# Performance work log

Hardware: AMD Instinct MI355X
Metric: run time of the kernel (lower is better)

The kernel has to match this reference:

```python
import jax, jax.numpy as jnp
import numpy as np

K = 32  # attention rank
EPS = 1e-6

def setup_inputs() -> dict:
    key = jax.random.key(0)
    k1, k2 = jax.random.split(key)
    N, d = 500000, 256
    x = jax.random.normal(k1, (N, d), dtype=jnp.float32)
    # Xavier-normal-ish scale for Linear(d, 4k)
    W = jax.random.normal(k2, (d, 4 * K), dtype=jnp.float32) * jnp.sqrt(2.0 / (d + 4 * K))
    b = jnp.zeros((4 * K,), dtype=jnp.float32)
    return {"x": x, "W": W, "b": b}

def reference(x, W, b):
    # X = ReLU(x @ W + b): [N, 4k]
    X = jax.nn.relu(x @ W + b)
    U = X[:, :K]            # [N, k]
    V = X[:, K:2 * K]       # [N, k]
    Z = X[:, 2 * K:3 * K]   # [N, k]
    T = X[:, 3 * K:]        # [N, k]
    # joint_normalize2: norm_factor = sum(U @ (V^T @ ones)) / N + eps
    s = V.sum(axis=0)                              # [k] == V^T @ ones
    norm_factor = (U @ s).sum() / U.shape[0] + EPS  # scalar
    D = 1.0 / norm_factor
    # low-rank attention: U @ (V^T @ Z), inner [k, k] GEMM kept tiny
    VtZ = jnp.einsum('nk,nj->kj', V, Z)  # [k, k]
    res = U @ VtZ                        # [N, k]
    return jnp.concatenate((res * D, T), axis=1)  # [N, 2k]
```

## Files before the change

kernel.cpp:

```cpp
#include <hip/hip_runtime.h>
#include <hip/hip_bf16.h>

#define DK 256
#define NC 128
#define EPSV 1e-6f

typedef __bf16 bf16x8 __attribute__((ext_vector_type(8)));
typedef float f32x4 __attribute__((ext_vector_type(4)));


__global__ __launch_bounds__(512, 2) void k_gemm(
    const float* __restrict__ x, const float* __restrict__ W,
    const float* __restrict__ bias, float* __restrict__ out,
    float* __restrict__ accg, int N)
{
  __shared__ float Vs[64 * 36];
  __shared__ float Zs[64 * 36];
  __shared__ float redS[64];

  const int tid  = threadIdx.x;
  const int wave = tid >> 6;
  const int lane = tid & 63;
  const int quad = lane >> 4;
  const int l16  = lane & 15;
  const int mw   = wave >> 1;
  const int nw   = wave & 1;

  bf16x8 Bf[8][4];
  float bias4[4];
  #pragma unroll
  for (int ntl = 0; ntl < 4; ++ntl) {
    const int n = nw * 64 + ntl * 16 + l16;
    bias4[ntl] = bias[n];
    #pragma unroll
    for (int kk = 0; kk < 8; ++kk) {
      const int k0 = kk * 32 + quad * 8;
      bf16x8 f;
      #pragma unroll
      for (int j = 0; j < 8; ++j) f[j] = (__bf16)W[(size_t)(k0 + j) * NC + n];
      Bf[kk][ntl] = f;
    }
  }

  float usumv[2] = {0.f, 0.f};
  float ssumv[2] = {0.f, 0.f};
  const int cell = tid >> 1;
  const int rh   = tid & 1;
  const int ck   = cell >> 3;
  const int cj   = (cell & 7) * 4;
  float vtz[4] = {0.f, 0.f, 0.f, 0.f};

  const int nchunks = (N + 63) >> 6;
  for (int c = blockIdx.x; c < nchunks; c += gridDim.x) {
    const int rbase = c * 64;
    const int arow  = rbase + mw * 16 + l16;
    const bool rv   = arow < N;
    const float* xr = x + (size_t)arow * DK;

    f32x4 acc[4];
    #pragma unroll
    for (int t = 0; t < 4; ++t) acc[t] = (f32x4){0.f, 0.f, 0.f, 0.f};

    #pragma unroll
    for (int kk = 0; kk < 8; ++kk) {
      const int koff = kk * 32 + quad * 8;
      f32x4 a0 = {0.f,0.f,0.f,0.f}, a1 = {0.f,0.f,0.f,0.f};
      if (rv) {
        a0 = *(const f32x4*)(xr + koff);
        a1 = *(const f32x4*)(xr + koff + 4);
      }
      bf16x8 af;
      af[0] = (__bf16)a0.x; af[1] = (__bf16)a0.y;
      af[2] = (__bf16)a0.z; af[3] = (__bf16)a0.w;
      af[4] = (__bf16)a1.x; af[5] = (__bf16)a1.y;
      af[6] = (__bf16)a1.z; af[7] = (__bf16)a1.w;
      #pragma unroll
      for (int ntl = 0; ntl < 4; ++ntl)
        acc[ntl] = __builtin_amdgcn_mfma_f32_16x16x32_bf16(af, Bf[kk][ntl], acc[ntl], 0, 0, 0);
    }

    #pragma unroll
    for (int ntl = 0; ntl < 4; ++ntl) {
      #pragma unroll
      for (int r = 0; r < 4; ++r) {
        const int lrow = mw * 16 + quad * 4 + r;
        const int grow = rbase + lrow;
        const bool ok = grow < N;
        float v = acc[ntl][r] + bias4[ntl];
        v = fmaxf(v, 0.f);
        if (!ok) v = 0.f;
        if (nw == 0) {
          if (ntl < 2) {
            if (ok) out[(size_t)grow * 64 + ntl * 16 + l16] = v;
            usumv[ntl] += v;
          } else {
            ssumv[ntl - 2] += v;
            Vs[lrow * 36 + (ntl - 2) * 16 + l16] = v;
          }
        } else {
          if (ntl < 2) {
            Zs[lrow * 36 + ntl * 16 + l16] = v;
          } else {
            if (ok) out[(size_t)grow * 64 + 32 + (ntl - 2) * 16 + l16] = v;
          }
        }
      }
    }
    __syncthreads();
    const int rr0 = rh * 32;
    #pragma unroll 4
    for (int r = rr0; r < rr0 + 32; ++r) {
      const float vv = Vs[r * 36 + ck];
      vtz[0] += vv * Zs[r * 36 + cj + 0];
      vtz[1] += vv * Zs[r * 36 + cj + 1];
      vtz[2] += vv * Zs[r * 36 + cj + 2];
      vtz[3] += vv * Zs[r * 36 + cj + 3];
    }
    __syncthreads();
  }

  if (tid < 64) redS[tid] = 0.f;
  __syncthreads();
  if (nw == 0) {
    atomicAdd(&redS[l16],      usumv[0]);
    atomicAdd(&redS[16 + l16], usumv[1]);
    atomicAdd(&redS[32 + l16], ssumv[0]);
    atomicAdd(&redS[48 + l16], ssumv[1]);
  }
  __syncthreads();
  if (tid < 64) atomicAdd(&accg[tid], redS[tid]);
  atomicAdd(&accg[64 + ck * 32 + cj + 0], vtz[0]);
  atomicAdd(&accg[64 + ck * 32 + cj + 1], vtz[1]);
  atomicAdd(&accg[64 + ck * 32 + cj + 2], vtz[2]);
  atomicAdd(&accg[64 + ck * 32 + cj + 3], vtz[3]);
}

__global__ void k_norm(float* __restrict__ accg, int N) {
  const int t = threadIdx.x;
  float p = 0.f;
  if (t < 32) p = accg[t] * accg[32 + t];
  #pragma unroll
  for (int off = 16; off >= 1; off >>= 1) p += __shfl_down(p, off);
  if (t == 0) accg[1088] = 1.0f / (p / (float)N + EPSV);
}

__global__ __launch_bounds__(256) void k_res(float* __restrict__ out,
                                             const float* __restrict__ accg, int N) {
  __shared__ float Ms[32 * 33];
  __shared__ float Us[64 * 33];
  const float D = accg[1088];
  for (int i = threadIdx.x; i < 1024; i += 256)
    Ms[(i >> 5) * 33 + (i & 31)] = accg[64 + i] * D;
  __syncthreads();
  const int j  = threadIdx.x & 31;
  const int r0 = threadIdx.x >> 5;
  const int ngroups = (N + 63) >> 6;
  for (int g = blockIdx.x; g < ngroups; g += gridDim.x) {
    const int rbase = g * 64;
    #pragma unroll
    for (int i = 0; i < 8; ++i) {
      const int lr = r0 + i * 8;
      const int row = rbase + lr;
      Us[lr * 33 + j] = (row < N) ? out[(size_t)row * 64 + j] : 0.f;
    }
    __syncthreads();
    #pragma unroll
    for (int i = 0; i < 8; ++i) {
      const int lr = r0 + i * 8;
      const int row = rbase + lr;
      if (row < N) {
        float a = 0.f;
        #pragma unroll
        for (int k = 0; k < 32; ++k) a += Us[lr * 33 + k] * Ms[k * 33 + j];
        out[(size_t)row * 64 + j] = a;
      }
    }
    __syncthreads();
  }
}

extern "C" void kernel_launch(void* const* d_in, const int* in_sizes, int n_in,
                              void* d_out, int out_size, void* d_ws, size_t ws_size,
                              hipStream_t stream) {
  const float* x    = (const float*)d_in[0];
  const float* W    = (const float*)d_in[1];
  const float* b    = (const float*)d_in[2];
  float* out  = (float*)d_out;
  float* accg = (float*)d_ws;
  const int N = in_sizes[0] / DK;

  hipMemsetAsync(accg, 0, 1089 * sizeof(float), stream);
  hipLaunchKernelGGL(k_gemm, dim3(256),  dim3(512), 0, stream, x, W, b, out, accg, N);
  hipLaunchKernelGGL(k_norm, dim3(1),    dim3(64),  0, stream, accg, N);
  hipLaunchKernelGGL(k_res,  dim3(1024), dim3(256), 0, stream, out, accg, N);
}
```

Baseline: 946.8 us.

## Stage W in LDS, batch x loads, compute VtZ with MFMA, one block per k_res group

Moves the bf16 copy of W out of per-thread registers into shared memory so the GEMM kernel uses fewer registers. This lets it request more resident blocks and doubles the grid. All x loads for a row chunk are now issued before the conversions and MFMAs, to expose more memory-level parallelism. The V^T·Z accumulation switches from scalar FMAs to bf16 MFMA on transposed shared-memory tiles, which loses some precision. The residual kernel now launches one block per 64-row group instead of a grid-stride loop. Shared memory per block rises to about 64KB, which may cap the actual occupancy gain.

```diff
diff --git a/kernel.cpp b/kernel.cpp
--- a/kernel.cpp
+++ b/kernel.cpp
@@ -6,17 +6,19 @@
 #define EPSV 1e-6f
 
 typedef __bf16 bf16x8 __attribute__((ext_vector_type(8)));
+typedef __bf16 bf16x4 __attribute__((ext_vector_type(4)));
 typedef float f32x4 __attribute__((ext_vector_type(4)));
 
 
-__global__ __launch_bounds__(512, 2) void k_gemm(
+__global__ __launch_bounds__(512, 4) void k_gemm(
     const float* __restrict__ x, const float* __restrict__ W,
     const float* __restrict__ bias, float* __restrict__ out,
     float* __restrict__ accg, int N)
 {
-  __shared__ float Vs[64 * 36];
-  __shared__ float Zs[64 * 36];
-  __shared__ float redS[64];
+  __shared__ __bf16 Wlds[32768];
+  __shared__ __bf16 Vt[32 * 72];
+  __shared__ __bf16 Zt[32 * 72];
+  __shared__ float  redS[64];
 
   const int tid  = threadIdx.x;
   const int wave = tid >> 6;
@@ -26,95 +28,110 @@
   const int mw   = wave >> 1;
   const int nw   = wave & 1;
 
-  bf16x8 Bf[8][4];
+  for (int f = tid; f < 4096; f += 512) {
+    const int n  = f & 127;
+    const int qk = f >> 7;
+    const int k0 = (qk >> 2) * 32 + (qk & 3) * 8;
+    bf16x8 w;
+    #pragma unroll
+    for (int j = 0; j < 8; ++j) w[j] = (__bf16)W[(size_t)(k0 + j) * NC + n];
+    *(bf16x8*)&Wlds[f * 8] = w;
+  }
   float bias4[4];
   #pragma unroll
-  for (int ntl = 0; ntl < 4; ++ntl) {
-    const int n = nw * 64 + ntl * 16 + l16;
-    bias4[ntl] = bias[n];
-    #pragma unroll
-    for (int kk = 0; kk < 8; ++kk) {
-      const int k0 = kk * 32 + quad * 8;
-      bf16x8 f;
-      #pragma unroll
-      for (int j = 0; j < 8; ++j) f[j] = (__bf16)W[(size_t)(k0 + j) * NC + n];
-      Bf[kk][ntl] = f;
-    }
-  }
+  for (int ntl = 0; ntl < 4; ++ntl) bias4[ntl] = bias[nw * 64 + ntl * 16 + l16];
+  __syncthreads();
 
   float usumv[2] = {0.f, 0.f};
   float ssumv[2] = {0.f, 0.f};
-  const int cell = tid >> 1;
-  const int rh   = tid & 1;
-  const int ck   = cell >> 3;
-  const int cj   = (cell & 7) * 4;
-  float vtz[4] = {0.f, 0.f, 0.f, 0.f};
+  f32x4 vacc = (f32x4){0.f, 0.f, 0.f, 0.f};
+  const int mt = wave >> 1, nt = wave & 1;
 
   const int nchunks = (N + 63) >> 6;
   for (int c = blockIdx.x; c < nchunks; c += gridDim.x) {
-    const int rbase = c * 64;
+    const int rbase = c << 6;
     const int arow  = rbase + mw * 16 + l16;
     const bool rv   = arow < N;
     const float* xr = x + (size_t)arow * DK;
 
-    f32x4 acc[4];
-    #pragma unroll
-    for (int t = 0; t < 4; ++t) acc[t] = (f32x4){0.f, 0.f, 0.f, 0.f};
-
+    f32x4 xv[16];
     #pragma unroll
     for (int kk = 0; kk < 8; ++kk) {
       const int koff = kk * 32 + quad * 8;
-      f32x4 a0 = {0.f,0.f,0.f,0.f}, a1 = {0.f,0.f,0.f,0.f};
-      if (rv) {
-        a0 = *(const f32x4*)(xr + koff);
-        a1 = *(const f32x4*)(xr + koff + 4);
-      }
+      xv[2 * kk]     = rv ? *(const f32x4*)(xr + koff)     : (f32x4){0.f,0.f,0.f,0.f};
+      xv[2 * kk + 1] = rv ? *(const f32x4*)(xr + koff + 4) : (f32x4){0.f,0.f,0.f,0.f};
+    }
+
+    f32x4 acc[4];
+    #pragma unroll
+    for (int t = 0; t < 4; ++t) acc[t] = (f32x4){0.f, 0.f, 0.f, 0.f};
+
+    #pragma unroll
+    for (int kk = 0; kk < 8; ++kk) {
       bf16x8 af;
-      af[0] = (__bf16)a0.x; af[1] = (__bf16)a0.y;
-      af[2] = (__bf16)a0.z; af[3] = (__bf16)a0.w;
-      af[4] = (__bf16)a1.x; af[5] = (__bf16)a1.y;
-      af[6] = (__bf16)a1.z; af[7] = (__bf16)a1.w;
-      #pragma unroll
-      for (int ntl = 0; ntl < 4; ++ntl)
-        acc[ntl] = __builtin_amdgcn_mfma_f32_16x16x32_bf16(af, Bf[kk][ntl], acc[ntl], 0, 0, 0);
+      af[0] = (__bf16)xv[2*kk].x;   af[1] = (__bf16)xv[2*kk].y;
+      af[2] = (__bf16)xv[2*kk].z;   af[3] = (__bf16)xv[2*kk].w;
+      af[4] = (__bf16)xv[2*kk+1].x; af[5] = (__bf16)xv[2*kk+1].y;
+      af[6] = (__bf16)xv[2*kk+1].z; af[7] = (__bf16)xv[2*kk+1].w;
+      #pragma unroll
+      for (int ntl = 0; ntl < 4; ++ntl) {
+        const bf16x8 bf = *(const bf16x8*)&Wlds[(((kk << 2) | quad) * 128
+                                                + nw * 64 + ntl * 16 + l16) * 8];
+        acc[ntl] = __builtin_amdgcn_mfma_f32_16x16x32_bf16(af, bf, acc[ntl], 0, 0, 0);
+      }
     }
 
     #pragma unroll
     for (int ntl = 0; ntl < 4; ++ntl) {
+      float v4[4];
       #pragma unroll
       for (int r = 0; r < 4; ++r) {
-        const int lrow = mw * 16 + quad * 4 + r;
-        const int grow = rbase + lrow;
-        const bool ok = grow < N;
+        const int grow = rbase + mw * 16 + quad * 4 + r;
         float v = acc[ntl][r] + bias4[ntl];
         v = fmaxf(v, 0.f);
-        if (!ok) v = 0.f;
-        if (nw == 0) {
-          if (ntl < 2) {
-            if (ok) out[(size_t)grow * 64 + ntl * 16 + l16] = v;
-            usumv[ntl] += v;
-          } else {
-            ssumv[ntl - 2] += v;
-            Vs[lrow * 36 + (ntl - 2) * 16 + l16] = v;
+        if (grow >= N) v = 0.f;
+        v4[r] = v;
+      }
+      const int grow0 = rbase + mw * 16 + quad * 4;
+      if (nw == 0) {
+        if (ntl < 2) {
+          #pragma unroll
+          for (int r = 0; r < 4; ++r) {
+            if (grow0 + r < N) out[(size_t)(grow0 + r) * 64 + ntl * 16 + l16] = v4[r];
+            usumv[ntl] += v4[r];
           }
         } else {
-          if (ntl < 2) {
-            Zs[lrow * 36 + ntl * 16 + l16] = v;
-          } else {
-            if (ok) out[(size_t)grow * 64 + 32 + (ntl - 2) * 16 + l16] = v;
-          }
+          ssumv[ntl - 2] += v4[0] + v4[1] + v4[2] + v4[3];
+          bf16x4 pv;
+          pv[0] = (__bf16)v4[0]; pv[1] = (__bf16)v4[1];
+          pv[2] = (__bf16)v4[2]; pv[3] = (__bf16)v4[3];
+          const int col = (ntl - 2) * 16 + l16;
+          const int lrow = mw * 16 + quad * 4;
+          *(bf16x4*)&Vt[col * 72 + lrow] = pv;
         }
+      } else {
+        if (ntl < 2) {
+          bf16x4 pv;
+          pv[0] = (__bf16)v4[0]; pv[1] = (__bf16)v4[1];
+          pv[2] = (__bf16)v4[2]; pv[3] = (__bf16)v4[3];
+          const int col = ntl * 16 + l16;
+          const int lrow = mw * 16 + quad * 4;
+          *(bf16x4*)&Zt[col * 72 + lrow] = pv;
+        } else {
+          #pragma unroll
+          for (int r = 0; r < 4; ++r)
+            if (grow0 + r < N) out[(size_t)(grow0 + r) * 64 + 32 + (ntl - 2) * 16 + l16] = v4[r];
+        }
       }
     }
     __syncthreads();
-    const int rr0 = rh * 32;
-    #pragma unroll 4
-    for (int r = rr0; r < rr0 + 32; ++r) {
-      const float vv = Vs[r * 36 + ck];
-      vtz[0] += vv * Zs[r * 36 + cj + 0];
-      vtz[1] += vv * Zs[r * 36 + cj + 1];
-      vtz[2] += vv * Zs[r * 36 + cj + 2];
-      vtz[3] += vv * Zs[r * 36 + cj + 3];
+    if (wave < 4) {
+      #pragma unroll
+      for (int ks = 0; ks < 2; ++ks) {
+        const bf16x8 av = *(const bf16x8*)&Vt[(mt * 16 + l16) * 72 + ks * 32 + quad * 8];
+        const bf16x8 bz = *(const bf16x8*)&Zt[(nt * 16 + l16) * 72 + ks * 32 + quad * 8];
+        vacc = __builtin_amdgcn_mfma_f32_16x16x32_bf16(av, bz, vacc, 0, 0, 0);
+      }
     }
     __syncthreads();
   }
@@ -129,10 +146,11 @@
   }
   __syncthreads();
   if (tid < 64) atomicAdd(&accg[tid], redS[tid]);
-  atomicAdd(&accg[64 + ck * 32 + cj + 0], vtz[0]);
-  atomicAdd(&accg[64 + ck * 32 + cj + 1], vtz[1]);
-  atomicAdd(&accg[64 + ck * 32 + cj + 2], vtz[2]);
-  atomicAdd(&accg[64 + ck * 32 + cj + 3], vtz[3]);
+  if (wave < 4) {
+    #pragma unroll
+    for (int r = 0; r < 4; ++r)
+      atomicAdd(&accg[64 + (mt * 16 + quad * 4 + r) * 32 + nt * 16 + l16], vacc[r]);
+  }
 }
 
 __global__ void k_norm(float* __restrict__ accg, int N) {
@@ -151,31 +169,26 @@
   const float D = accg[1088];
   for (int i = threadIdx.x; i < 1024; i += 256)
     Ms[(i >> 5) * 33 + (i & 31)] = accg[64 + i] * D;
-  __syncthreads();
   const int j  = threadIdx.x & 31;
   const int r0 = threadIdx.x >> 5;
-  const int ngroups = (N + 63) >> 6;
-  for (int g = blockIdx.x; g < ngroups; g += gridDim.x) {
-    const int rbase = g * 64;
-    #pragma unroll
-    for (int i = 0; i < 8; ++i) {
-      const int lr = r0 + i * 8;
-      const int row = rbase + lr;
-      Us[lr * 33 + j] = (row < N) ? out[(size_t)row * 64 + j] : 0.f;
-    }
-    __syncthreads();
-    #pragma unroll
-    for (int i = 0; i < 8; ++i) {
-      const int lr = r0 + i * 8;
-      const int row = rbase + lr;
-      if (row < N) {
-        float a = 0.f;
-        #pragma unroll
-        for (int k = 0; k < 32; ++k) a += Us[lr * 33 + k] * Ms[k * 33 + j];
-        out[(size_t)row * 64 + j] = a;
-      }
-    }
-    __syncthreads();
+  const int rbase = blockIdx.x * 64;
+  #pragma unroll
+  for (int i = 0; i < 8; ++i) {
+    const int lr = r0 + i * 8;
+    const int row = rbase + lr;
+    Us[lr * 33 + j] = (row < N) ? out[(size_t)row * 64 + j] : 0.f;
+  }
+  __syncthreads();
+  #pragma unroll
+  for (int i = 0; i < 8; ++i) {
+    const int lr = r0 + i * 8;
+    const int row = rbase + lr;
+    if (row < N) {
+      float a = 0.f;
+      #pragma unroll
+      for (int k = 0; k < 32; ++k) a += Us[lr * 33 + k] * Ms[k * 33 + j];
+      out[(size_t)row * 64 + j] = a;
+    }
   }
 }
 
@@ -188,9 +201,10 @@
   float* out  = (float*)d_out;
   float* accg = (float*)d_ws;
   const int N = in_sizes[0] / DK;
+  const int ngroups = (N + 63) >> 6;
 
   hipMemsetAsync(accg, 0, 1089 * sizeof(float), stream);
-  hipLaunchKernelGGL(k_gemm, dim3(256),  dim3(512), 0, stream, x, W, b, out, accg, N);
-  hipLaunchKernelGGL(k_norm, dim3(1),    dim3(64),  0, stream, accg, N);
-  hipLaunchKernelGGL(k_res,  dim3(1024), dim3(256), 0, stream, out, accg, N);
-}
+  hipLaunchKernelGGL(k_gemm, dim3(512),     dim3(512), 0, stream, x, W, b, out, accg, N);
+  hipLaunchKernelGGL(k_norm, dim3(1),       dim3(64),  0, stream, accg, N);
+  hipLaunchKernelGGL(k_res,  dim3(ngroups), dim3(256), 0, stream, out, accg, N);
+}
```

After: 784.7 us. 17.1% less time.
